# Kernel tuning notes

Measured on AMD Instinct MI355X. Metric: run time of the kernel, lower is better.

The kernel has to match this reference:

```python
import jax, jax.numpy as jnp
import numpy as np

N, E, DIN, DOUT = 50000, 625000, 128, 128


def setup_inputs() -> dict:
    key = jax.random.key(0)
    k = jax.random.split(key, 4)
    x = jax.random.normal(k[0], (N, DIN), dtype=jnp.float32)
    edge_index = jax.random.randint(k[1], (2, E), 0, N, dtype=jnp.int32)
    s = 1.0 / np.sqrt(DIN)  # Glorot-ish init like torch Linear
    W_fwd = jax.random.uniform(k[2], (DIN, DOUT), jnp.float32, -s, s)
    W_bwd = jax.random.uniform(k[3], (DIN, DOUT), jnp.float32, -s, s)
    b_fwd = jnp.zeros((DOUT,), jnp.float32)
    b_bwd = jnp.zeros((DOUT,), jnp.float32)
    return {"x": x, "edge_index": edge_index, "W_fwd": W_fwd, "b_fwd": b_fwd,
            "W_bwd": W_bwd, "b_bwd": b_bwd}


def gcn_conv(x, W, b, src, dst, n):
    """PyG GCNConv: add self-loops, symmetric degree norm, gather-scatter aggregate."""
    loops = jnp.arange(n, dtype=src.dtype)
    src2 = jnp.concatenate([src, loops])  # [E+N]
    dst2 = jnp.concatenate([dst, loops])
    ones = jnp.ones(src2.shape[0], dtype=x.dtype)
    deg = jax.ops.segment_sum(ones, dst2, num_segments=n)  # in-degree incl. self-loop
    dinv = jnp.where(deg > 0, jax.lax.rsqrt(deg), 0.0)
    norm = dinv[src2] * dinv[dst2]  # [E+N]
    h = x @ W  # [N, DOUT] dense GEMM before message passing
    msgs = h[src2] * norm[:, None]  # gather + scale, [E+N, DOUT]
    out = jax.ops.segment_sum(msgs, dst2, num_segments=n)  # scatter-add
    return out + b


def reference(x, edge_index, W_fwd, b_fwd, W_bwd, b_bwd):
    src, dst = edge_index[0], edge_index[1]
    n = x.shape[0]
    x_forward = gcn_conv(x, W_fwd, b_fwd, src, dst, n)
    # reversed edge direction for the backward diffusion conv
    x_backward = gcn_conv(x, W_bwd, b_bwd, dst, src, n)
    # dropout omitted (eval mode / deterministic reference)
    return jax.nn.relu(x_forward + x_backward)
```

## Files before the change

kernel.cpp:

```cpp
#include <hip/hip_runtime.h>
#include <hip/hip_bf16.h>
#include <cstdint>

static constexpr int BLK      = 256;
static constexpr int CAP      = 40;
static constexpr int BINSHIFT = 8;
static constexpr int BINNODES = 1 << BINSHIFT;
static constexpr int BINCAP   = BINNODES * CAP / 2;
static constexpr int EPB      = 1024;
static constexpr int OVMAX    = 1024;
static constexpr int NB2MAX   = 512;

typedef __attribute__((ext_vector_type(8))) short bf16x8;
typedef __attribute__((ext_vector_type(4))) float f32x4;

__device__ __forceinline__ float bf16lo(uint32_t u) { return __uint_as_float(u << 16); }
__device__ __forceinline__ float bf16hi(uint32_t u) { return __uint_as_float(u & 0xffff0000u); }
__device__ __forceinline__ float bf16f(unsigned short u) { return __uint_as_float((uint32_t)u << 16); }
__device__ __forceinline__ unsigned short f2bf(float f) {
    __hip_bfloat16 h = __float2bfloat16(f);
    return *(unsigned short*)&h;
}

__global__ __launch_bounds__(BLK) void k_bin_conv(
        const int* __restrict__ src, const int* __restrict__ dst, int ne,
        uint32_t* __restrict__ pair, int* __restrict__ gcnt,
        int* __restrict__ ovcnt, int* __restrict__ ovlist, int nbins, int gbin,
        const float* __restrict__ x, uint32_t* __restrict__ xb32, int nxw, int gxc,
        const float* __restrict__ Wf, const float* __restrict__ Wb,
        unsigned short* __restrict__ WTf, unsigned short* __restrict__ WTb) {
    const int bid = blockIdx.x, tid = threadIdx.x;
    if (bid < gbin) {
        __shared__ uint32_t stage[EPB * 2];
        __shared__ unsigned short binof[EPB * 2];
        __shared__ int hist[NB2MAX];
        __shared__ int lofs[NB2MAX];
        __shared__ int gbase[NB2MAX];
        __shared__ int chunk[NB2MAX / 8];
        const int nb2 = 2 * nbins;
        for (int i = tid; i < nb2; i += BLK) hist[i] = 0;
        __syncthreads();

        int s[4], d[4];
        const int e0 = bid * EPB + tid;
#pragma unroll
        for (int k = 0; k < 4; ++k) {
            int e = e0 + k * BLK;
            bool v = e < ne;
            s[k] = v ? src[e] : -1;
            d[k] = v ? dst[e] : -1;
            if (v) {
                atomicAdd(&hist[d[k] >> BINSHIFT], 1);
                atomicAdd(&hist[nbins + (s[k] >> BINSHIFT)], 1);
            }
        }
        __syncthreads();

        const int nch = (nb2 + 7) >> 3;
        if (tid < nch) {
            int a = 0, base = tid << 3;
#pragma unroll
            for (int k = 0; k < 8; ++k) { int idx = base + k; if (idx < nb2) a += hist[idx]; }
            chunk[tid] = a;
        }
        __syncthreads();
        if (tid == 0) { int a = 0; for (int c = 0; c < nch; ++c) { int t = chunk[c]; chunk[c] = a; a += t; } }
        __syncthreads();
        for (int i = tid; i < nb2; i += BLK) {
            int a = chunk[i >> 3];
            for (int k = (i >> 3) << 3; k < i; ++k) a += hist[k];
            lofs[i] = a;
        }
        __syncthreads();
        for (int i = tid; i < nb2; i += BLK) {
            int c = hist[i];
            gbase[i] = c ? atomicAdd(&gcnt[i], c) : 0;
            hist[i] = lofs[i];
        }
        __syncthreads();
#pragma unroll
        for (int k = 0; k < 4; ++k) {
            if (s[k] >= 0) {
                int b0 = d[k] >> BINSHIFT;
                int p0 = atomicAdd(&hist[b0], 1);
                stage[p0] = ((uint32_t)d[k] << 16) | (uint32_t)s[k];
                binof[p0] = (unsigned short)b0;
                int b1 = nbins + (s[k] >> BINSHIFT);
                int p1 = atomicAdd(&hist[b1], 1);
                stage[p1] = ((uint32_t)s[k] << 16) | (uint32_t)d[k];
                binof[p1] = (unsigned short)b1;
            }
        }
        __syncthreads();
        int nval = ne - bid * EPB; if (nval > EPB) nval = EPB; if (nval < 0) nval = 0;
        const int total = 2 * nval;
        for (int i = tid; i < total; i += BLK) {
            int b = binof[i];
            int gidx = gbase[b] + (i - lofs[b]);
            if (gidx < BINCAP)
                pair[(size_t)b * BINCAP + gidx] = stage[i];
            else {
                int node = (int)(stage[i] >> 16);
                int q = atomicAdd(ovcnt, 1);
                if (q < OVMAX) ovlist[q] = (node << 1) | (b >= nbins ? 1 : 0);
            }
        }
        return;
    }
    if (bid < gbin + gxc) {
        int base = (bid - gbin) * 2048;
        int end = base + 2048; if (end > nxw) end = nxw;
        for (int i = base + tid; i < end; i += BLK) {
            float2 v = ((const float2*)x)[i];
            xb32[i] = ((uint32_t)f2bf(v.y) << 16) | (uint32_t)f2bf(v.x);
        }
        return;
    }
    int wb = bid - gbin - gxc;
    for (int idx = wb * 2048 + tid; idx < (wb + 1) * 2048; idx += BLK) {
        int c = idx >> 7, k = idx & 127;
        WTf[c * 128 + k] = f2bf(Wf[k * 128 + c]);
        WTb[c * 128 + k] = f2bf(Wb[k * 128 + c]);
    }
}

__global__ __launch_bounds__(BLK) void k_build(
        uint32_t* __restrict__ pair, const int* __restrict__ gcnt,
        int* __restrict__ cnt_f, int* __restrict__ cnt_b,
        float* __restrict__ dinv_f, float* __restrict__ dinv_b,
        int* __restrict__ ovcnt, int* __restrict__ ovlist,
        int n, int nbins) {
    const int bid = blockIdx.x, tid = threadIdx.x;
    __shared__ unsigned short buck[BINNODES * CAP];
    __shared__ int lcnt[BINNODES];
    lcnt[tid] = 0;
    __syncthreads();
    int count = gcnt[bid]; if (count > BINCAP) count = BINCAP;
    const uint32_t* pb = pair + (size_t)bid * BINCAP;
    const int dir = bid >= nbins ? 1 : 0;
    for (int i = tid; i < count; i += BLK) {
        uint32_t p = pb[i];
        int l = (p >> 16) & (BINNODES - 1);
        int r = atomicAdd(&lcnt[l], 1);
        if (r < CAP) buck[l * CAP + r] = (unsigned short)(p & 0xffffu);
        else {
            int q = atomicAdd(ovcnt, 1);
            if (q < OVMAX)
                ovlist[q] = (((((bid - dir * nbins) << BINSHIFT) + l)) << 1) | dir;
        }
    }
    __syncthreads();
    const int node = ((bid - dir * nbins) << BINSHIFT) + tid;
    if (node < n) {
        int c = lcnt[tid];
        if (dir) { cnt_b[node] = c; dinv_b[node] = rsqrtf(1.0f + (float)c); }
        else     { cnt_f[node] = c; dinv_f[node] = rsqrtf(1.0f + (float)c); }
    }
    uint32_t* seg = pair + (size_t)bid * BINCAP;
    const uint32_t* b32 = (const uint32_t*)buck;
    for (int i = tid; i < BINCAP; i += BLK) seg[i] = b32[i];
}

__device__ __forceinline__ void accum_range(
        int j0, int j1, int ofs, float sc,
        const uint32_t* __restrict__ xb, int lane, float& a0, float& a1) {
    int j = j0;
    for (; j + 8 <= j1; j += 8) {
        int   o0 = __shfl(ofs, j + 0), o1 = __shfl(ofs, j + 1);
        int   o2 = __shfl(ofs, j + 2), o3 = __shfl(ofs, j + 3);
        int   o4 = __shfl(ofs, j + 4), o5 = __shfl(ofs, j + 5);
        int   o6 = __shfl(ofs, j + 6), o7 = __shfl(ofs, j + 7);
        float s0 = __shfl(sc, j + 0), s1 = __shfl(sc, j + 1);
        float s2 = __shfl(sc, j + 2), s3 = __shfl(sc, j + 3);
        float s4 = __shfl(sc, j + 4), s5 = __shfl(sc, j + 5);
        float s6 = __shfl(sc, j + 6), s7 = __shfl(sc, j + 7);
        uint32_t u0 = xb[(size_t)(o0 + lane)], u1 = xb[(size_t)(o1 + lane)];
        uint32_t u2 = xb[(size_t)(o2 + lane)], u3 = xb[(size_t)(o3 + lane)];
        uint32_t u4 = xb[(size_t)(o4 + lane)], u5 = xb[(size_t)(o5 + lane)];
        uint32_t u6 = xb[(size_t)(o6 + lane)], u7 = xb[(size_t)(o7 + lane)];
        a0 = fmaf(s0, bf16lo(u0), a0); a1 = fmaf(s0, bf16hi(u0), a1);
        a0 = fmaf(s1, bf16lo(u1), a0); a1 = fmaf(s1, bf16hi(u1), a1);
        a0 = fmaf(s2, bf16lo(u2), a0); a1 = fmaf(s2, bf16hi(u2), a1);
        a0 = fmaf(s3, bf16lo(u3), a0); a1 = fmaf(s3, bf16hi(u3), a1);
        a0 = fmaf(s4, bf16lo(u4), a0); a1 = fmaf(s4, bf16hi(u4), a1);
        a0 = fmaf(s5, bf16lo(u5), a0); a1 = fmaf(s5, bf16hi(u5), a1);
        a0 = fmaf(s6, bf16lo(u6), a0); a1 = fmaf(s6, bf16hi(u6), a1);
        a0 = fmaf(s7, bf16lo(u7), a0); a1 = fmaf(s7, bf16hi(u7), a1);
    }
    for (; j + 4 <= j1; j += 4) {
        int   o0 = __shfl(ofs, j + 0), o1 = __shfl(ofs, j + 1);
        int   o2 = __shfl(ofs, j + 2), o3 = __shfl(ofs, j + 3);
        float s0 = __shfl(sc, j + 0), s1 = __shfl(sc, j + 1);
        float s2 = __shfl(sc, j + 2), s3 = __shfl(sc, j + 3);
        uint32_t u0 = xb[(size_t)(o0 + lane)], u1 = xb[(size_t)(o1 + lane)];
        uint32_t u2 = xb[(size_t)(o2 + lane)], u3 = xb[(size_t)(o3 + lane)];
        a0 = fmaf(s0, bf16lo(u0), a0); a1 = fmaf(s0, bf16hi(u0), a1);
        a0 = fmaf(s1, bf16lo(u1), a0); a1 = fmaf(s1, bf16hi(u1), a1);
        a0 = fmaf(s2, bf16lo(u2), a0); a1 = fmaf(s2, bf16hi(u2), a1);
        a0 = fmaf(s3, bf16lo(u3), a0); a1 = fmaf(s3, bf16hi(u3), a1);
    }
    for (; j < j1; ++j) {
        int oj = __shfl(ofs, j); float sj = __shfl(sc, j);
        uint32_t uj = xb[(size_t)(oj + lane)];
        a0 = fmaf(sj, bf16lo(uj), a0); a1 = fmaf(sj, bf16hi(uj), a1);
    }
}

__global__ __launch_bounds__(BLK) void k_gather_gemm(
        const int* __restrict__ cnt_f, const int* __restrict__ cnt_b,
        const unsigned short* __restrict__ adj_f,
        const unsigned short* __restrict__ adj_b,
        const float* __restrict__ dinv_f, const float* __restrict__ dinv_b,
        const uint32_t* __restrict__ xb32,
        const unsigned short* __restrict__ WTf,
        const unsigned short* __restrict__ WTb,
        const float* __restrict__ bfv, const float* __restrict__ bbv,
        float* __restrict__ out, int n, int gnode2,
        const int* __restrict__ ovcnt, const int* __restrict__ ovlist,
        const int* __restrict__ src, const int* __restrict__ dst, int ne) {
    __shared__ uint32_t aggL[16 * 132];
    __shared__ int ovflag[16];
    __shared__ int lst[2048];
    __shared__ int lc;
    const int bid = blockIdx.x, tid = threadIdx.x;
    if (bid < gnode2) {
        const int wave = tid >> 6, lane = tid & 63;
        const int node0 = bid * 16;
        for (int i4 = 0; i4 < 4; ++i4) {
            const int row = wave * 4 + i4;
            const int node = node0 + row;
            int cf = 0, cb = 0;
            bool skip = node >= n;
            if (!skip) { cf = cnt_f[node]; cb = cnt_b[node]; skip = (cf > CAP || cb > CAP); }
            if (lane == 0) ovflag[row] = skip ? 1 : 0;
            if (skip) continue;

            float dvsf = dinv_f[node], dvsb = dinv_b[node];
            uint32_t uv = xb32[(size_t)node * 64 + lane];
            float accf0 = dvsf * dvsf * bf16lo(uv), accf1 = dvsf * dvsf * bf16hi(uv);
            float accb0 = dvsb * dvsb * bf16lo(uv), accb1 = dvsb * dvsb * bf16hi(uv);

            const int mt = cf + cb;
            if (mt <= 64) {
                int ofs = 0; float sc = 0.f;
                if (lane < cf) {
                    int nb = adj_f[node * CAP + lane];
                    ofs = nb * 64;
                    sc  = dvsf * dinv_f[nb];
                } else if (lane < mt) {
                    int nb = adj_b[node * CAP + (lane - cf)];
                    ofs = nb * 64;
                    sc  = dvsb * dinv_b[nb];
                }
                accum_range(0,  cf, ofs, sc, xb32, lane, accf0, accf1);
                accum_range(cf, mt, ofs, sc, xb32, lane, accb0, accb1);
            } else {
                for (int j = 0; j < cf; ++j) {
                    int nb = adj_f[node * CAP + j];
                    float dj = dvsf * dinv_f[nb];
                    uint32_t u = xb32[(size_t)nb * 64 + lane];
                    accf0 = fmaf(dj, bf16lo(u), accf0); accf1 = fmaf(dj, bf16hi(u), accf1);
                }
                for (int j = 0; j < cb; ++j) {
                    int nb = adj_b[node * CAP + j];
                    float dj = dvsb * dinv_b[nb];
                    uint32_t u = xb32[(size_t)nb * 64 + lane];
                    accb0 = fmaf(dj, bf16lo(u), accb0); accb1 = fmaf(dj, bf16hi(u), accb1);
                }
            }
            aggL[row * 132 + lane] =
                ((uint32_t)f2bf(accf1) << 16) | (uint32_t)f2bf(accf0);
            aggL[row * 132 + 64 + lane] =
                ((uint32_t)f2bf(accb1) << 16) | (uint32_t)f2bf(accb0);
        }
        __syncthreads();

        const int q = lane >> 4, t16 = lane & 15;
        bf16x8 a[8];
#pragma unroll
        for (int s = 0; s < 8; ++s)
            a[s] = *(const bf16x8*)((const char*)aggL + t16 * 528 + s * 64 + q * 16);
#pragma unroll
        for (int t2 = 0; t2 < 2; ++t2) {
            const int col = (wave * 2 + t2) * 16 + t16;
            const unsigned short* wrf = WTf + (size_t)col * 128;
            const unsigned short* wrb = WTb + (size_t)col * 128;
            f32x4 c = {0.f, 0.f, 0.f, 0.f};
#pragma unroll
            for (int s = 0; s < 4; ++s)
                c = __builtin_amdgcn_mfma_f32_16x16x32_bf16(
                        a[s], *(const bf16x8*)(wrf + s * 32 + q * 8), c, 0, 0, 0);
#pragma unroll
            for (int s = 0; s < 4; ++s)
                c = __builtin_amdgcn_mfma_f32_16x16x32_bf16(
                        a[4 + s], *(const bf16x8*)(wrb + s * 32 + q * 8), c, 0, 0, 0);
            const float bias = bfv[col] + bbv[col];
#pragma unroll
            for (int r = 0; r < 4; ++r) {
                int row = q * 4 + r;
                int node = node0 + row;
                if (node < n && !ovflag[row])
                    out[(size_t)node * 128 + col] = fmaxf(c[r] + bias, 0.f);
            }
        }
        return;
    }

    int nov = *ovcnt; if (nov > OVMAX) nov = OVMAX;
    if (nov == 0) return;
    float* aggfl = (float*)aggL;
    for (int i = bid - gnode2; i < nov; i += 8) {
        int node = ovlist[i] >> 1;
        for (int d2 = 0; d2 < 2; ++d2) {
            const int* key = d2 ? src : dst;
            const int* val = d2 ? dst : src;
            const float* dinv = d2 ? dinv_b : dinv_f;
            float dvs = dinv[node];
            float s0 = 0.f, s1 = 0.f;
            if (tid < 64) {
                uint32_t u = xb32[(size_t)node * 64 + tid];
                s0 = dvs * bf16lo(u); s1 = dvs * bf16hi(u);
            }
            for (int start = 0; start < ne; start += 2048) {
                if (tid == 0) lc = 0;
                __syncthreads();
                int end = min(start + 2048, ne);
                for (int e2 = start + tid; e2 < end; e2 += BLK)
                    if (key[e2] == node) { int qq = atomicAdd(&lc, 1); lst[qq] = val[e2]; }
                __syncthreads();
                int mm = lc;
                if (tid < 64) {
                    for (int j = 0; j < mm; ++j) {
                        int nb = lst[j];
                        float dv = dinv[nb];
                        uint32_t u = xb32[(size_t)nb * 64 + tid];
                        s0 = fmaf(dv, bf16lo(u), s0);
                        s1 = fmaf(dv, bf16hi(u), s1);
                    }
                }
                __syncthreads();
            }
            if (tid < 64) {
                aggfl[d2 * 128 + 2 * tid]     = bf16f(f2bf(dvs * s0));
                aggfl[d2 * 128 + 2 * tid + 1] = bf16f(f2bf(dvs * s1));
            }
            __syncthreads();
        }
        if (tid < 128) {
            const int col = tid;
            float acc = bfv[col] + bbv[col];
            const unsigned short* wrf = WTf + (size_t)col * 128;
            const unsigned short* wrb = WTb + (size_t)col * 128;
            for (int k = 0; k < 128; ++k) {
                acc = fmaf(aggfl[k],       bf16f(wrf[k]), acc);
                acc = fmaf(aggfl[128 + k], bf16f(wrb[k]), acc);
            }
            out[(size_t)node * 128 + col] = fmaxf(acc, 0.f);
        }
        __syncthreads();
    }
}

extern "C" void kernel_launch(void* const* d_in, const int* in_sizes, int n_in,
                              void* d_out, int out_size, void* d_ws, size_t ws_size,
                              hipStream_t stream) {
    const float* x  = (const float*)d_in[0];
    const int*   ei = (const int*)d_in[1];
    const float* Wf = (const float*)d_in[2];
    const float* bf = (const float*)d_in[3];
    const float* Wb = (const float*)d_in[4];
    const float* bb = (const float*)d_in[5];

    const int n  = in_sizes[0] / 128;
    const int ne = in_sizes[1] / 2;
    const int* src = ei;
    const int* dst = ei + ne;
    float* out = (float*)d_out;

    const int nbins = (n + BINNODES - 1) >> BINSHIFT;
    const int nb2   = 2 * nbins;

    char* w = (char*)d_ws;
    uint32_t* pair = (uint32_t*)w;              w += (size_t)nb2 * BINCAP * 4;
    uint32_t* xb32 = (uint32_t*)w;              w += (size_t)n * 64 * 4;
    float* dinv_f = (float*)w;                  w += (size_t)n * 4;
    float* dinv_b = (float*)w;                  w += (size_t)n * 4;
    unsigned short* WTf = (unsigned short*)w;   w += 128 * 128 * 2;
    unsigned short* WTb = (unsigned short*)w;   w += 128 * 128 * 2;
    int* cnt_f = (int*)w;                       w += (size_t)n * 4;
    int* cnt_b = (int*)w;                       w += (size_t)n * 4;
    int* gcnt = (int*)w;                        w += (size_t)nb2 * 4;
    int* ovcnt = (int*)w;                       w += 8 * 4;
    int* ovlist = (int*)w;                      w += OVMAX * 4;

    const unsigned short* adj_f = (const unsigned short*)pair;
    const unsigned short* adj_b = adj_f + (size_t)nbins * BINNODES * CAP;

    const int gbin   = (ne + EPB - 1) / EPB;
    const int gxc    = (n * 64 + 2047) / 2048;
    const int gnode2 = (n + 15) / 16;

    hipMemsetAsync(gcnt, 0, (size_t)(nb2 + 8) * 4, stream);

    k_bin_conv<<<gbin + gxc + 8, BLK, 0, stream>>>(src, dst, ne,
                                                   pair, gcnt, ovcnt, ovlist,
                                                   nbins, gbin,
                                                   x, xb32, n * 64, gxc,
                                                   Wf, Wb, WTf, WTb);

    k_build<<<nb2, BLK, 0, stream>>>(pair, gcnt, cnt_f, cnt_b,
                                     dinv_f, dinv_b, ovcnt, ovlist, n, nbins);

    k_gather_gemm<<<gnode2 + 8, BLK, 0, stream>>>(cnt_f, cnt_b, adj_f, adj_b,
                                                  dinv_f, dinv_b, xb32,
                                                  WTf, WTb, bf, bb,
                                                  out, n, gnode2,
                                                  ovcnt, ovlist, src, dst, ne);
}
```

Measured before the change: 181.0 us.

## Use 1024-thread blocks with one wave per node in gather-GEMM kernel

The gather-GEMM kernel now launches 16 waves per block, so each wave aggregates a single node instead of looping over four. Only the first 8 waves then run the MFMA tile, one 16-column slice each, and the A fragments are read straight from LDS rather than preloaded. The aim is more memory-level parallelism during the latency-bound neighbour gathers. The costs are half the waves idling during the GEMM phase, larger blocks that are harder to schedule, and an overflow path whose stride now assumes 1024 threads.

```diff
diff --git a/kernel.cpp b/kernel.cpp
--- a/kernel.cpp
+++ b/kernel.cpp
@@ -206,7 +206,7 @@
     }
 }
 
-__global__ __launch_bounds__(BLK) void k_gather_gemm(
+__global__ __launch_bounds__(1024, 8) void k_gather_gemm(
         const int* __restrict__ cnt_f, const int* __restrict__ cnt_b,
         const unsigned short* __restrict__ adj_f,
         const unsigned short* __restrict__ adj_b,
@@ -225,16 +225,14 @@
     const int bid = blockIdx.x, tid = threadIdx.x;
     if (bid < gnode2) {
         const int wave = tid >> 6, lane = tid & 63;
-        const int node0 = bid * 16;
-        for (int i4 = 0; i4 < 4; ++i4) {
-            const int row = wave * 4 + i4;
-            const int node = node0 + row;
-            int cf = 0, cb = 0;
-            bool skip = node >= n;
-            if (!skip) { cf = cnt_f[node]; cb = cnt_b[node]; skip = (cf > CAP || cb > CAP); }
-            if (lane == 0) ovflag[row] = skip ? 1 : 0;
-            if (skip) continue;
-
+        const int node = bid * 16 + wave;
+
+        int cf = 0, cb = 0;
+        bool skip = node >= n;
+        if (!skip) { cf = cnt_f[node]; cb = cnt_b[node]; skip = (cf > CAP || cb > CAP); }
+        if (lane == 0) ovflag[wave] = skip ? 1 : 0;
+
+        if (!skip) {
             float dvsf = dinv_f[node], dvsb = dinv_b[node];
             uint32_t uv = xb32[(size_t)node * 64 + lane];
             float accf0 = dvsf * dvsf * bf16lo(uv), accf1 = dvsf * dvsf * bf16hi(uv);
@@ -268,39 +266,37 @@
                     accb0 = fmaf(dj, bf16lo(u), accb0); accb1 = fmaf(dj, bf16hi(u), accb1);
                 }
             }
-            aggL[row * 132 + lane] =
+            aggL[wave * 132 + lane] =
                 ((uint32_t)f2bf(accf1) << 16) | (uint32_t)f2bf(accf0);
-            aggL[row * 132 + 64 + lane] =
+            aggL[wave * 132 + 64 + lane] =
                 ((uint32_t)f2bf(accb1) << 16) | (uint32_t)f2bf(accb0);
         }
         __syncthreads();
 
-        const int q = lane >> 4, t16 = lane & 15;
-        bf16x8 a[8];
-#pragma unroll
-        for (int s = 0; s < 8; ++s)
-            a[s] = *(const bf16x8*)((const char*)aggL + t16 * 528 + s * 64 + q * 16);
-#pragma unroll
-        for (int t2 = 0; t2 < 2; ++t2) {
-            const int col = (wave * 2 + t2) * 16 + t16;
+        if (wave < 8) {
+            const int q = lane >> 4, t16 = lane & 15;
+            const int col = wave * 16 + t16;
+            const char* arow = (const char*)aggL + t16 * 528;
             const unsigned short* wrf = WTf + (size_t)col * 128;
             const unsigned short* wrb = WTb + (size_t)col * 128;
             f32x4 c = {0.f, 0.f, 0.f, 0.f};
 #pragma unroll
             for (int s = 0; s < 4; ++s)
                 c = __builtin_amdgcn_mfma_f32_16x16x32_bf16(
-                        a[s], *(const bf16x8*)(wrf + s * 32 + q * 8), c, 0, 0, 0);
+                        *(const bf16x8*)(arow + s * 64 + q * 16),
+                        *(const bf16x8*)(wrf + s * 32 + q * 8), c, 0, 0, 0);
 #pragma unroll
             for (int s = 0; s < 4; ++s)
                 c = __builtin_amdgcn_mfma_f32_16x16x32_bf16(
-                        a[4 + s], *(const bf16x8*)(wrb + s * 32 + q * 8), c, 0, 0, 0);
+                        *(const bf16x8*)(arow + 256 + s * 64 + q * 16),
+                        *(const bf16x8*)(wrb + s * 32 + q * 8), c, 0, 0, 0);
             const float bias = bfv[col] + bbv[col];
 #pragma unroll
             for (int r = 0; r < 4; ++r) {
                 int row = q * 4 + r;
-                int node = node0 + row;
-                if (node < n && !ovflag[row])
-                    out[(size_t)node * 128 + col] = fmaxf(c[r] + bias, 0.f);
+                int node2 = bid * 16 + row;
+                if (node2 < n && !ovflag[row])
+                    out[(size_t)node2 * 128 + col] = fmaxf(c[r] + bias, 0.f);
             }
         }
         return;
@@ -325,7 +321,7 @@
                 if (tid == 0) lc = 0;
                 __syncthreads();
                 int end = min(start + 2048, ne);
-                for (int e2 = start + tid; e2 < end; e2 += BLK)
+                for (int e2 = start + tid; e2 < end; e2 += 1024)
                     if (key[e2] == node) { int qq = atomicAdd(&lc, 1); lst[qq] = val[e2]; }
                 __syncthreads();
                 int mm = lc;
@@ -411,9 +407,9 @@
     k_build<<<nb2, BLK, 0, stream>>>(pair, gcnt, cnt_f, cnt_b,
                                      dinv_f, dinv_b, ovcnt, ovlist, n, nbins);
 
-    k_gather_gemm<<<gnode2 + 8, BLK, 0, stream>>>(cnt_f, cnt_b, adj_f, adj_b,
-                                                  dinv_f, dinv_b, xb32,
-                                                  WTf, WTb, bf, bb,
-                                                  out, n, gnode2,
-                                                  ovcnt, ovlist, src, dst, ne);
-}
+    k_gather_gemm<<<gnode2 + 8, 1024, 0, stream>>>(cnt_f, cnt_b, adj_f, adj_b,
+                                                   dinv_f, dinv_b, xb32,
+                                                   WTf, WTb, bf, bb,
+                                                   out, n, gnode2,
+                                                   ovcnt, ovlist, src, dst, ne);
+}
```

Result: slower. 185.3 us (+2.4%).

## Shrink gather-GEMM LDS, let last-finishing wave do GEMM, double binning edges per block

Applied to the files above, without the earlier changes.

The gather/GEMM kernel now places the adjacency list buffer and the aggregate tile in one shared-memory union and raises the occupancy hint via launch bounds. This cuts LDS use so more blocks can be resident at once. The block-wide barrier before the MFMA stage is replaced by an LDS atomic counter: only the last wave to finish aggregating computes all 8 column tiles, and the other waves exit early. The binning kernel also processes 2048 edges per block instead of 1024. The cost is that one wave now serialises the GEMM that four waves used to share.

```diff
diff --git a/kernel.cpp b/kernel.cpp
--- a/kernel.cpp
+++ b/kernel.cpp
@@ -7,7 +7,7 @@
 static constexpr int BINSHIFT = 8;
 static constexpr int BINNODES = 1 << BINSHIFT;
 static constexpr int BINCAP   = BINNODES * CAP / 2;
-static constexpr int EPB      = 1024;
+static constexpr int EPB      = 2048;
 static constexpr int OVMAX    = 1024;
 static constexpr int NB2MAX   = 512;
 
@@ -41,10 +41,10 @@
         for (int i = tid; i < nb2; i += BLK) hist[i] = 0;
         __syncthreads();
 
-        int s[4], d[4];
+        int s[8], d[8];
         const int e0 = bid * EPB + tid;
 #pragma unroll
-        for (int k = 0; k < 4; ++k) {
+        for (int k = 0; k < 8; ++k) {
             int e = e0 + k * BLK;
             bool v = e < ne;
             s[k] = v ? src[e] : -1;
@@ -79,7 +79,7 @@
         }
         __syncthreads();
 #pragma unroll
-        for (int k = 0; k < 4; ++k) {
+        for (int k = 0; k < 8; ++k) {
             if (s[k] >= 0) {
                 int b0 = d[k] >> BINSHIFT;
                 int p0 = atomicAdd(&hist[b0], 1);
@@ -206,7 +206,7 @@
     }
 }
 
-__global__ __launch_bounds__(BLK) void k_gather_gemm(
+__global__ __launch_bounds__(BLK, 8) void k_gather_gemm(
         const int* __restrict__ cnt_f, const int* __restrict__ cnt_b,
         const unsigned short* __restrict__ adj_f,
         const unsigned short* __restrict__ adj_b,
@@ -218,14 +218,18 @@
         float* __restrict__ out, int n, int gnode2,
         const int* __restrict__ ovcnt, const int* __restrict__ ovlist,
         const int* __restrict__ src, const int* __restrict__ dst, int ne) {
-    __shared__ uint32_t aggL[16 * 132];
+    __shared__ __align__(16) char smemU[16 * 528];
     __shared__ int ovflag[16];
-    __shared__ int lst[2048];
+    __shared__ int donec;
     __shared__ int lc;
     const int bid = blockIdx.x, tid = threadIdx.x;
     if (bid < gnode2) {
+        uint32_t* aggL = (uint32_t*)smemU;
         const int wave = tid >> 6, lane = tid & 63;
         const int node0 = bid * 16;
+        if (tid == 0) donec = 0;
+        __syncthreads();
+
         for (int i4 = 0; i4 < 4; ++i4) {
             const int row = wave * 4 + i4;
             const int node = node0 + row;
@@ -273,16 +277,23 @@
             aggL[row * 132 + 64 + lane] =
                 ((uint32_t)f2bf(accb1) << 16) | (uint32_t)f2bf(accb0);
         }
-        __syncthreads();
+
+        __threadfence_block();
+        int prev = 0;
+        if (lane == 0) prev = atomicAdd(&donec, 1);
+        prev = __shfl(prev, 0);
+        if (prev != 3) return;
+        __threadfence_block();
 
         const int q = lane >> 4, t16 = lane & 15;
+        const char* arow = smemU + t16 * 528;
         bf16x8 a[8];
 #pragma unroll
         for (int s = 0; s < 8; ++s)
-            a[s] = *(const bf16x8*)((const char*)aggL + t16 * 528 + s * 64 + q * 16);
-#pragma unroll
-        for (int t2 = 0; t2 < 2; ++t2) {
-            const int col = (wave * 2 + t2) * 16 + t16;
+            a[s] = *(const bf16x8*)(arow + s * 64 + q * 16);
+#pragma unroll
+        for (int t = 0; t < 8; ++t) {
+            const int col = t * 16 + t16;
             const unsigned short* wrf = WTf + (size_t)col * 128;
             const unsigned short* wrb = WTb + (size_t)col * 128;
             f32x4 c = {0.f, 0.f, 0.f, 0.f};
@@ -298,9 +309,9 @@
 #pragma unroll
             for (int r = 0; r < 4; ++r) {
                 int row = q * 4 + r;
-                int node = node0 + row;
-                if (node < n && !ovflag[row])
-                    out[(size_t)node * 128 + col] = fmaxf(c[r] + bias, 0.f);
+                int node2 = node0 + row;
+                if (node2 < n && !ovflag[row])
+                    out[(size_t)node2 * 128 + col] = fmaxf(c[r] + bias, 0.f);
             }
         }
         return;
@@ -308,7 +319,9 @@
 
     int nov = *ovcnt; if (nov > OVMAX) nov = OVMAX;
     if (nov == 0) return;
-    float* aggfl = (float*)aggL;
+    int* lst = (int*)smemU;
+    float* aggfl = (float*)(smemU);
+    __shared__ float afix[256];
     for (int i = bid - gnode2; i < nov; i += 8) {
         int node = ovlist[i] >> 1;
         for (int d2 = 0; d2 < 2; ++d2) {
@@ -341,8 +354,8 @@
                 __syncthreads();
             }
             if (tid < 64) {
-                aggfl[d2 * 128 + 2 * tid]     = bf16f(f2bf(dvs * s0));
-                aggfl[d2 * 128 + 2 * tid + 1] = bf16f(f2bf(dvs * s1));
+                afix[d2 * 128 + 2 * tid]     = bf16f(f2bf(dvs * s0));
+                afix[d2 * 128 + 2 * tid + 1] = bf16f(f2bf(dvs * s1));
             }
             __syncthreads();
         }
@@ -352,12 +365,13 @@
             const unsigned short* wrf = WTf + (size_t)col * 128;
             const unsigned short* wrb = WTb + (size_t)col * 128;
             for (int k = 0; k < 128; ++k) {
-                acc = fmaf(aggfl[k],       bf16f(wrf[k]), acc);
-                acc = fmaf(aggfl[128 + k], bf16f(wrb[k]), acc);
+                acc = fmaf(afix[k],       bf16f(wrf[k]), acc);
+                acc = fmaf(afix[128 + k], bf16f(wrb[k]), acc);
             }
             out[(size_t)node * 128 + col] = fmaxf(acc, 0.f);
         }
         __syncthreads();
+        (void)aggfl;
     }
 }
 
```

Measured after the change: 177.4 us. -2.0%, faster.
